# Optimization experiments

Measured on AMD Instinct MI355X. Metric: run time of the kernel, lower is better.

The kernel has to match this reference:

```python
import jax, jax.numpy as jnp
import numpy as np
from jax import lax

K = 3
STRIDE = 1
PAD = 1


def setup_inputs() -> dict:
    key = jax.random.key(0)
    k0, k1, k2, k3 = jax.random.split(key, 4)
    B, C, H, W, O = 8, 128, 64, 64, 128
    x = jax.random.normal(k0, (B, C, H, W), jnp.float32)
    # offset_conv: Conv2d(C, 2*K*K) - small init so sampled offsets stay moderate
    w_off = jax.random.normal(k1, (2 * K * K, C, K, K), jnp.float32) * 0.01
    b_off = jnp.zeros((2 * K * K,), jnp.float32)
    # deform_conv main weight, kaiming-ish scale
    w_def = jax.random.normal(k2, (O, C, K, K), jnp.float32) * (1.0 / np.sqrt(C * K * K))
    b_def = jax.random.normal(k3, (O,), jnp.float32) * 0.01
    return {"x": x, "w_off": w_off, "b_off": b_off, "w_def": w_def, "b_def": b_def}


def _conv2d(x, w, b, stride, pad):
    y = lax.conv_general_dilated(
        x, w, window_strides=(stride, stride), padding=[(pad, pad), (pad, pad)],
        dimension_numbers=("NCHW", "OIHW", "NCHW"))
    return y + b[None, :, None, None]


def _bilinear_sample(x, py, px):
    """x: [B,C,Hin,Win]; py,px: [B,KK,H,W] -> [B,C,KK,H,W] with zero padding."""
    B, C, Hin, Win = x.shape
    iy0f = jnp.floor(py)
    ix0f = jnp.floor(px)
    wy = py - iy0f  # grad of floor is 0, so d(wy)/d(py) = 1 (matches deform conv)
    wx = px - ix0f
    iy0 = iy0f.astype(jnp.int32)
    ix0 = ix0f.astype(jnp.int32)

    def gather(iy, ix):
        valid = (iy >= 0) & (iy < Hin) & (ix >= 0) & (ix < Win)
        iyc = jnp.clip(iy, 0, Hin - 1)
        ixc = jnp.clip(ix, 0, Win - 1)
        g = jax.vmap(lambda xb, a, b: xb[:, a, b])(x, iyc, ixc)  # [B,C,KK,H,W]
        return g * valid[:, None].astype(x.dtype)

    v00 = gather(iy0, ix0)
    v01 = gather(iy0, ix0 + 1)
    v10 = gather(iy0 + 1, ix0)
    v11 = gather(iy0 + 1, ix0 + 1)
    wy_ = wy[:, None]
    wx_ = wx[:, None]
    return (v00 * (1 - wy_) * (1 - wx_) + v01 * (1 - wy_) * wx_
            + v10 * wy_ * (1 - wx_) + v11 * wy_ * wx_)


def reference(x, w_off, b_off, w_def, b_def):
    B, C, H, W = x.shape
    O = w_def.shape[0]
    KK = K * K
    # 1) standard conv predicting offsets: [B, 2*KK, Hout, Wout]
    offsets = _conv2d(x, w_off, b_off, STRIDE, PAD)
    Hout, Wout = offsets.shape[2], offsets.shape[3]
    # torchvision layout: interleaved (dy, dx) per kernel tap
    off = offsets.reshape(B, KK, 2, Hout, Wout)
    off_y, off_x = off[:, :, 0], off[:, :, 1]  # [B,KK,Hout,Wout]
    # 2) base sampling grid per kernel tap
    kys, kxs = jnp.meshgrid(jnp.arange(K), jnp.arange(K), indexing="ij")
    kys = kys.reshape(KK).astype(jnp.float32)
    kxs = kxs.reshape(KK).astype(jnp.float32)
    hs = (jnp.arange(Hout) * STRIDE - PAD).astype(jnp.float32)
    ws = (jnp.arange(Wout) * STRIDE - PAD).astype(jnp.float32)
    base_y = hs[None, :, None] + kys[:, None, None]  # [KK,Hout,1]
    base_x = ws[None, None, :] + kxs[:, None, None]  # [KK,1,Wout]
    py = base_y[None] + off_y  # [B,KK,Hout,Wout]
    px = base_x[None] + off_x
    # 3) gather bilinear-sampled patches then dense contraction (im2col GEMM)
    sampled = _bilinear_sample(x, py, px)  # [B,C,KK,Hout,Wout]
    out = jnp.einsum("bckhw,ock->bohw", sampled, w_def.reshape(O, C, KK))
    return out + b_def[None, :, None, None]
```

## Files before the change

kernel.cpp:

```cpp
#include <hip/hip_runtime.h>

#define BB 8
#define CC 128
#define HH 64
#define WW 64
#define OO 128
#define NJ 18
#define HW 4096

typedef unsigned short u16;
typedef unsigned int u32;
typedef __attribute__((ext_vector_type(8))) __bf16 bf16x8;
typedef __attribute__((ext_vector_type(4))) float f32x4;

__device__ __forceinline__ u16 f2bf(float f) {
    u32 u = __float_as_uint(f);
    u += 0x7fffu + ((u >> 16) & 1u);
    return (u16)(u >> 16);
}
__device__ __forceinline__ float bflo(u32 u) { return __uint_as_float(u << 16); }
__device__ __forceinline__ float bfhi(u32 u) { return __uint_as_float(u & 0xffff0000u); }

__global__ __launch_bounds__(256)
void k_xT(const float* __restrict__ x, u16* __restrict__ xT) {
    __shared__ float tile[128][65];
    const int t = threadIdx.x;
    const int b = blockIdx.x >> 6;
    const int hw0 = (blockIdx.x & 63) << 6;
    const float* xb = x + (size_t)b * CC * HW + hw0;
    const int tw = t & 63, tc = t >> 6;
#pragma unroll
    for (int r = 0; r < 32; ++r) {
        int c = r * 4 + tc;
        tile[c][tw] = xb[c * HW + tw];
    }
    __syncthreads();
    const int seg = t & 15, hwl = t >> 4;
    u16* dst = xT + ((size_t)b * HW + hw0) * CC;
#pragma unroll
    for (int r = 0; r < 4; ++r) {
        int hw = hwl + r * 16;
        union { u16 u[8]; uint4 v; } p;
#pragma unroll
        for (int i = 0; i < 8; ++i) p.u[i] = f2bf(tile[seg * 8 + i][hw]);
        *(uint4*)&dst[hw * CC + seg * 8] = p.v;
    }
}

__global__ void k_prep(const float* __restrict__ w_def,
                       const float* __restrict__ w_off,
                       u16* __restrict__ wT, u16* __restrict__ wA) {
    int idx = blockIdx.x * 256 + threadIdx.x;
    if (idx < 9 * OO * CC) {
        int c = idx & 127, o = (idx >> 7) & 127, kk = idx >> 14;
        wT[idx] = f2bf(w_def[(o * CC + c) * 9 + kk]);
    }
    if (idx < 32 * 1152) {
        int k = idx % 1152, j = idx / 1152;
        int q = k >> 7, c = k & 127;
        wA[idx] = (j < NJ) ? f2bf(w_off[(j * CC + c) * 9 + q]) : (u16)0;
    }
}

__global__ __launch_bounds__(256, 2)
void k_off(const u16* __restrict__ xT, const u16* __restrict__ wA,
           const float* __restrict__ b_off, float* __restrict__ offs) {
    __shared__ u16 s_x[198 * 128];
    const int t = threadIdx.x, lane = t & 63, wv = t >> 6;
    const int posl = lane & 15, kg = lane >> 4;
    const int b = blockIdx.x >> 6, h = blockIdx.x & 63;

    for (int it = t; it < 3168; it += 256) {
        int seg = it & 15, pix = it >> 4;
        int r = pix / 66, wp = pix - r * 66;
        int y = h - 1 + r, w = wp - 1;
        uint4 v = make_uint4(0, 0, 0, 0);
        if (y >= 0 && y < HH && w >= 0 && w < WW)
            v = *(const uint4*)&xT[((size_t)(b * HW) + y * WW + w) * CC + seg * 8];
        *(uint4*)&s_x[pix * 128 + ((seg ^ (pix & 15)) * 8)] = v;
    }
    __syncthreads();

    f32x4 acc0 = {0.f, 0.f, 0.f, 0.f}, acc1 = {0.f, 0.f, 0.f, 0.f};
    for (int q = 0; q < 9; ++q) {
        int qy = q / 3, qx = q - qy * 3;
        int pix = qy * 66 + (wv * 16 + posl) + qx;
        int prow = pix * 128, pxor = pix & 15;
#pragma unroll
        for (int ki = 0; ki < 4; ++ki) {
            int ks = q * 4 + ki;
            int cidx = ki * 4 + kg;
            bf16x8 bfr = *(const bf16x8*)&s_x[prow + ((cidx ^ pxor) * 8)];
            bf16x8 a0 = *(const bf16x8*)&wA[posl * 1152 + ks * 32 + kg * 8];
            bf16x8 a1 = *(const bf16x8*)&wA[(16 + posl) * 1152 + ks * 32 + kg * 8];
            acc0 = __builtin_amdgcn_mfma_f32_16x16x32_bf16(a0, bfr, acc0, 0, 0, 0);
            acc1 = __builtin_amdgcn_mfma_f32_16x16x32_bf16(a1, bfr, acc1, 0, 0, 0);
        }
    }
    const int pos = wv * 16 + posl;
#pragma unroll
    for (int r = 0; r < 4; ++r) {
        int j = kg * 4 + r;
        offs[(b * NJ + j) * HW + h * WW + pos] = acc0[r] + b_off[j];
    }
#pragma unroll
    for (int r = 0; r < 4; ++r) {
        int j = 16 + kg * 4 + r;
        if (j < NJ) offs[(b * NJ + j) * HW + h * WW + pos] = acc1[r] + b_off[j];
    }
}

__global__ __launch_bounds__(256, 2)
void k_main(const u16* __restrict__ xT, const float* __restrict__ offs,
            const u16* __restrict__ wT, const float* __restrict__ b_def,
            float* __restrict__ out) {
    __shared__ u16    s_wt[128 * 128];
    __shared__ u16    s_samp[128 * 128];
    __shared__ float4 s_cw[128];
    __shared__ int4   s_co[128];

    const int t = threadIdx.x, lane = t & 63, wv = t >> 6;
    const int posl = lane & 15, rg = lane >> 4;
    const int b = blockIdx.x >> 5;
    const int h0 = (blockIdx.x & 31) << 1;
    const char* xb = (const char*)xT + (size_t)b * (HW * CC * 2);

    f32x4 acc[8][2];
#pragma unroll
    for (int mt = 0; mt < 8; ++mt) {
        acc[mt][0] = (f32x4){0.f, 0.f, 0.f, 0.f};
        acc[mt][1] = (f32x4){0.f, 0.f, 0.f, 0.f};
    }

    for (int kk = 0; kk < 9; ++kk) {
        if (t < 128) {
            int w = t & 63, hc = h0 + (t >> 6);
            int ky = kk / 3, kx = kk - ky * 3;
            int idy = (b * NJ + 2 * kk) * HW + hc * WW + w;
            float oy = offs[idy];
            float ox = offs[idy + HW];
            float py = (float)(hc - 1 + ky) + oy;
            float px = (float)(w - 1 + kx) + ox;
            float fy = floorf(py), fx = floorf(px);
            int iy0 = (int)fy, ix0 = (int)fx;
            float wy = py - fy, wx = px - fx;
            int iy1 = iy0 + 1, ix1 = ix0 + 1;
            float my0 = (iy0 >= 0 && iy0 < HH) ? 1.0f : 0.0f;
            float my1 = (iy1 >= 0 && iy1 < HH) ? 1.0f : 0.0f;
            float mx0 = (ix0 >= 0 && ix0 < WW) ? 1.0f : 0.0f;
            float mx1 = (ix1 >= 0 && ix1 < WW) ? 1.0f : 0.0f;
            int iy0c = min(max(iy0, 0), HH - 1), iy1c = min(max(iy1, 0), HH - 1);
            int ix0c = min(max(ix0, 0), WW - 1), ix1c = min(max(ix1, 0), WW - 1);
            float wy1 = 1.0f - wy, wx1 = 1.0f - wx;
            s_cw[t] = make_float4(my0 * mx0 * wy1 * wx1, my0 * mx1 * wy1 * wx,
                                  my1 * mx0 * wy  * wx1, my1 * mx1 * wy  * wx);
            s_co[t] = make_int4((iy0c * WW + ix0c) << 8, (iy0c * WW + ix1c) << 8,
                                (iy1c * WW + ix0c) << 8, (iy1c * WW + ix1c) << 8);
        }
        __syncthreads();

#pragma unroll
        for (int r = 0; r < 8; ++r) {
            int item = r * 256 + t;
            int o = item >> 4, sg = item & 15;
            *(uint4*)&s_wt[o * 128 + ((sg ^ (o & 15)) * 8)] =
                *(const uint4*)&wT[kk * (OO * CC) + item * 8];
        }
        {
            const int sg = t & 15;
            const char* base = xb + sg * 16;
#pragma unroll
            for (int r = 0; r < 8; ++r) {
                int pos = (t >> 4) + r * 16;
                float4 cw = s_cw[pos];
                int4 co = s_co[pos];
                uint4 q00 = *(const uint4*)(base + co.x);
                uint4 q01 = *(const uint4*)(base + co.y);
                uint4 q10 = *(const uint4*)(base + co.z);
                uint4 q11 = *(const uint4*)(base + co.w);
                const u32* u00 = (const u32*)&q00;
                const u32* u01 = (const u32*)&q01;
                const u32* u10 = (const u32*)&q10;
                const u32* u11 = (const u32*)&q11;
                union { u16 u[8]; uint4 v; } p;
#pragma unroll
                for (int i = 0; i < 4; ++i) {
                    float s0 = cw.x * bflo(u00[i]) + cw.y * bflo(u01[i])
                             + cw.z * bflo(u10[i]) + cw.w * bflo(u11[i]);
                    float s1 = cw.x * bfhi(u00[i]) + cw.y * bfhi(u01[i])
                             + cw.z * bfhi(u10[i]) + cw.w * bfhi(u11[i]);
                    p.u[2 * i]     = f2bf(s0);
                    p.u[2 * i + 1] = f2bf(s1);
                }
                *(uint4*)&s_samp[pos * 128 + ((sg ^ (pos & 15)) * 8)] = p.v;
            }
        }
        __syncthreads();

#pragma unroll
        for (int ct = 0; ct < 4; ++ct) {
            const int cidx = ct * 4 + rg;
            const int sw = (cidx ^ posl) * 8;
            bf16x8 bf0 = *(const bf16x8*)&s_samp[(2 * wv * 16 + posl) * 128 + sw];
            bf16x8 bf1 = *(const bf16x8*)&s_samp[((2 * wv + 1) * 16 + posl) * 128 + sw];
#pragma unroll
            for (int mt = 0; mt < 8; ++mt) {
                bf16x8 af = *(const bf16x8*)&s_wt[(mt * 16 + posl) * 128 + sw];
                acc[mt][0] = __builtin_amdgcn_mfma_f32_16x16x32_bf16(af, bf0, acc[mt][0], 0, 0, 0);
                acc[mt][1] = __builtin_amdgcn_mfma_f32_16x16x32_bf16(af, bf1, acc[mt][1], 0, 0, 0);
            }
        }
        __syncthreads();
    }

#pragma unroll
    for (int mt = 0; mt < 8; ++mt) {
#pragma unroll
        for (int j = 0; j < 2; ++j) {
            int pos = (2 * wv + j) * 16 + posl;
            int h = h0 + (pos >> 6), w = pos & 63;
#pragma unroll
            for (int r = 0; r < 4; ++r) {
                int o = mt * 16 + rg * 4 + r;
                out[((b * OO + o) * HH + h) * WW + w] = acc[mt][j][r] + b_def[o];
            }
        }
    }
}

extern "C" void kernel_launch(void* const* d_in, const int* in_sizes, int n_in,
                              void* d_out, int out_size, void* d_ws, size_t ws_size,
                              hipStream_t stream) {
    const float* x     = (const float*)d_in[0];
    const float* w_off = (const float*)d_in[1];
    const float* b_off = (const float*)d_in[2];
    const float* w_def = (const float*)d_in[3];
    const float* b_def = (const float*)d_in[4];
    float* out = (float*)d_out;

    float* offs = (float*)d_ws;
    u16*   xT   = (u16*)(offs + BB * NJ * HW);
    u16*   wT   = xT + (size_t)BB * HW * CC;
    u16*   wA   = wT + 9 * OO * CC;

    k_xT  <<<512, 256, 0, stream>>>(x, xT);
    k_prep<<<576, 256, 0, stream>>>(w_def, w_off, wT, wA);
    k_off <<<512, 256, 0, stream>>>(xT, wA, b_off, offs);
    k_main<<<256, 256, 0, stream>>>(xT, offs, wT, b_def, out);
}
```

Baseline: 139.4 us.

## Retile deformable conv to one row per block and compute sampling per lane

The main kernel now handles one output row (64 pixels) per block instead of two, doubling the grid to 512 blocks and raising launch bounds to 3 blocks per SM. Each lane computes its own bilinear coefficients inline, which removes the shared coefficient staging and one barrier per tap. The sample buffer is padded and relaid per channel segment. Separately, the transpose kernel changes its shared tile layout and packs bf16 pairs with a hardware conversion, and both offset and main kernels interleave batch in block index order to improve L2 locality. The trade-off is that the weight tile is reloaded to LDS for half as many pixels per block, doubling that traffic, and every wave recomputes the same sampling coefficients redundantly.

```diff
diff --git a/kernel.cpp b/kernel.cpp
--- a/kernel.cpp
+++ b/kernel.cpp
@@ -1,4 +1,5 @@
 #include <hip/hip_runtime.h>
+#include <hip/hip_bf16.h>
 
 #define BB 8
 #define CC 128
@@ -20,10 +21,15 @@
 }
 __device__ __forceinline__ float bflo(u32 u) { return __uint_as_float(u << 16); }
 __device__ __forceinline__ float bfhi(u32 u) { return __uint_as_float(u & 0xffff0000u); }
+__device__ __forceinline__ u32 pk2bf(float s0, float s1) {
+    union { __hip_bfloat162 h; u32 u; } cv;
+    cv.h = __float22bfloat162_rn(make_float2(s0, s1));
+    return cv.u;
+}
 
 __global__ __launch_bounds__(256)
 void k_xT(const float* __restrict__ x, u16* __restrict__ xT) {
-    __shared__ float tile[128][65];
+    __shared__ float tile[64][129];
     const int t = threadIdx.x;
     const int b = blockIdx.x >> 6;
     const int hw0 = (blockIdx.x & 63) << 6;
@@ -32,17 +38,18 @@
 #pragma unroll
     for (int r = 0; r < 32; ++r) {
         int c = r * 4 + tc;
-        tile[c][tw] = xb[c * HW + tw];
+        tile[tw][c] = xb[c * HW + tw];
     }
     __syncthreads();
-    const int seg = t & 15, hwl = t >> 4;
     u16* dst = xT + ((size_t)b * HW + hw0) * CC;
 #pragma unroll
     for (int r = 0; r < 4; ++r) {
-        int hw = hwl + r * 16;
-        union { u16 u[8]; uint4 v; } p;
-#pragma unroll
-        for (int i = 0; i < 8; ++i) p.u[i] = f2bf(tile[seg * 8 + i][hw]);
+        int item = t + (r << 8);
+        int seg = item & 15, hw = item >> 4;
+        union { u32 d[4]; uint4 v; } p;
+#pragma unroll
+        for (int i = 0; i < 4; ++i)
+            p.d[i] = pk2bf(tile[hw][seg * 8 + 2 * i], tile[hw][seg * 8 + 2 * i + 1]);
         *(uint4*)&dst[hw * CC + seg * 8] = p.v;
     }
 }
@@ -68,7 +75,7 @@
     __shared__ u16 s_x[198 * 128];
     const int t = threadIdx.x, lane = t & 63, wv = t >> 6;
     const int posl = lane & 15, kg = lane >> 4;
-    const int b = blockIdx.x >> 6, h = blockIdx.x & 63;
+    const int b = blockIdx.x & 7, h = blockIdx.x >> 3;
 
     for (int it = t; it < 3168; it += 256) {
         int seg = it & 15, pix = it >> 4;
@@ -110,55 +117,25 @@
     }
 }
 
-__global__ __launch_bounds__(256, 2)
+__global__ __launch_bounds__(256, 3)
 void k_main(const u16* __restrict__ xT, const float* __restrict__ offs,
             const u16* __restrict__ wT, const float* __restrict__ b_def,
             float* __restrict__ out) {
-    __shared__ u16    s_wt[128 * 128];
-    __shared__ u16    s_samp[128 * 128];
-    __shared__ float4 s_cw[128];
-    __shared__ int4   s_co[128];
+    __shared__ u16 s_wt[128 * 128];
+    __shared__ u16 s_samp[16 * 520];
 
     const int t = threadIdx.x, lane = t & 63, wv = t >> 6;
     const int posl = lane & 15, rg = lane >> 4;
-    const int b = blockIdx.x >> 5;
-    const int h0 = (blockIdx.x & 31) << 1;
+    const int b = blockIdx.x & 7;
+    const int h = blockIdx.x >> 3;
+    const int w = lane;
     const char* xb = (const char*)xT + (size_t)b * (HW * CC * 2);
 
-    f32x4 acc[8][2];
-#pragma unroll
-    for (int mt = 0; mt < 8; ++mt) {
-        acc[mt][0] = (f32x4){0.f, 0.f, 0.f, 0.f};
-        acc[mt][1] = (f32x4){0.f, 0.f, 0.f, 0.f};
-    }
+    f32x4 acc[8];
+#pragma unroll
+    for (int mt = 0; mt < 8; ++mt) acc[mt] = (f32x4){0.f, 0.f, 0.f, 0.f};
 
     for (int kk = 0; kk < 9; ++kk) {
-        if (t < 128) {
-            int w = t & 63, hc = h0 + (t >> 6);
-            int ky = kk / 3, kx = kk - ky * 3;
-            int idy = (b * NJ + 2 * kk) * HW + hc * WW + w;
-            float oy = offs[idy];
-            float ox = offs[idy + HW];
-            float py = (float)(hc - 1 + ky) + oy;
-            float px = (float)(w - 1 + kx) + ox;
-            float fy = floorf(py), fx = floorf(px);
-            int iy0 = (int)fy, ix0 = (int)fx;
-            float wy = py - fy, wx = px - fx;
-            int iy1 = iy0 + 1, ix1 = ix0 + 1;
-            float my0 = (iy0 >= 0 && iy0 < HH) ? 1.0f : 0.0f;
-            float my1 = (iy1 >= 0 && iy1 < HH) ? 1.0f : 0.0f;
-            float mx0 = (ix0 >= 0 && ix0 < WW) ? 1.0f : 0.0f;
-            float mx1 = (ix1 >= 0 && ix1 < WW) ? 1.0f : 0.0f;
-            int iy0c = min(max(iy0, 0), HH - 1), iy1c = min(max(iy1, 0), HH - 1);
-            int ix0c = min(max(ix0, 0), WW - 1), ix1c = min(max(ix1, 0), WW - 1);
-            float wy1 = 1.0f - wy, wx1 = 1.0f - wx;
-            s_cw[t] = make_float4(my0 * mx0 * wy1 * wx1, my0 * mx1 * wy1 * wx,
-                                  my1 * mx0 * wy  * wx1, my1 * mx1 * wy  * wx);
-            s_co[t] = make_int4((iy0c * WW + ix0c) << 8, (iy0c * WW + ix1c) << 8,
-                                (iy1c * WW + ix0c) << 8, (iy1c * WW + ix1c) << 8);
-        }
-        __syncthreads();
-
 #pragma unroll
         for (int r = 0; r < 8; ++r) {
             int item = r * 256 + t;
@@ -166,64 +143,72 @@
             *(uint4*)&s_wt[o * 128 + ((sg ^ (o & 15)) * 8)] =
                 *(const uint4*)&wT[kk * (OO * CC) + item * 8];
         }
-        {
-            const int sg = t & 15;
-            const char* base = xb + sg * 16;
-#pragma unroll
-            for (int r = 0; r < 8; ++r) {
-                int pos = (t >> 4) + r * 16;
-                float4 cw = s_cw[pos];
-                int4 co = s_co[pos];
-                uint4 q00 = *(const uint4*)(base + co.x);
-                uint4 q01 = *(const uint4*)(base + co.y);
-                uint4 q10 = *(const uint4*)(base + co.z);
-                uint4 q11 = *(const uint4*)(base + co.w);
-                const u32* u00 = (const u32*)&q00;
-                const u32* u01 = (const u32*)&q01;
-                const u32* u10 = (const u32*)&q10;
-                const u32* u11 = (const u32*)&q11;
-                union { u16 u[8]; uint4 v; } p;
-#pragma unroll
-                for (int i = 0; i < 4; ++i) {
-                    float s0 = cw.x * bflo(u00[i]) + cw.y * bflo(u01[i])
-                             + cw.z * bflo(u10[i]) + cw.w * bflo(u11[i]);
-                    float s1 = cw.x * bfhi(u00[i]) + cw.y * bfhi(u01[i])
-                             + cw.z * bfhi(u10[i]) + cw.w * bfhi(u11[i]);
-                    p.u[2 * i]     = f2bf(s0);
-                    p.u[2 * i + 1] = f2bf(s1);
-                }
-                *(uint4*)&s_samp[pos * 128 + ((sg ^ (pos & 15)) * 8)] = p.v;
+        int ky = kk / 3, kx = kk - ky * 3;
+        float oy = offs[(b * NJ + 2 * kk) * HW + h * WW + w];
+        float ox = offs[(b * NJ + 2 * kk + 1) * HW + h * WW + w];
+        float py = (float)(h - 1 + ky) + oy;
+        float px = (float)(w - 1 + kx) + ox;
+        float fy = floorf(py), fx = floorf(px);
+        int iy0 = (int)fy, ix0 = (int)fx;
+        float wy = py - fy, wx = px - fx;
+        int iy1 = iy0 + 1, ix1 = ix0 + 1;
+        float my0 = (iy0 >= 0 && iy0 < HH) ? 1.0f : 0.0f;
+        float my1 = (iy1 >= 0 && iy1 < HH) ? 1.0f : 0.0f;
+        float mx0 = (ix0 >= 0 && ix0 < WW) ? 1.0f : 0.0f;
+        float mx1 = (ix1 >= 0 && ix1 < WW) ? 1.0f : 0.0f;
+        int iy0c = min(max(iy0, 0), HH - 1), iy1c = min(max(iy1, 0), HH - 1);
+        int ix0c = min(max(ix0, 0), WW - 1), ix1c = min(max(ix1, 0), WW - 1);
+        float wy1 = 1.0f - wy, wx1 = 1.0f - wx;
+        float cwx = my0 * mx0 * wy1 * wx1, cwy = my0 * mx1 * wy1 * wx;
+        float cwz = my1 * mx0 * wy * wx1,  cww = my1 * mx1 * wy * wx;
+        int cox = (iy0c * WW + ix0c) << 8, coy = (iy0c * WW + ix1c) << 8;
+        int coz = (iy1c * WW + ix0c) << 8, cow = (iy1c * WW + ix1c) << 8;
+
+#pragma unroll
+        for (int j = 0; j < 4; ++j) {
+            const int seg = 4 * wv + j;
+            const char* base = xb + seg * 16;
+            uint4 q00 = *(const uint4*)(base + cox);
+            uint4 q01 = *(const uint4*)(base + coy);
+            uint4 q10 = *(const uint4*)(base + coz);
+            uint4 q11 = *(const uint4*)(base + cow);
+            const u32* u00 = (const u32*)&q00;
+            const u32* u01 = (const u32*)&q01;
+            const u32* u10 = (const u32*)&q10;
+            const u32* u11 = (const u32*)&q11;
+            union { u32 d[4]; uint4 v; } p;
+#pragma unroll
+            for (int i = 0; i < 4; ++i) {
+                float s0 = cwx * bflo(u00[i]) + cwy * bflo(u01[i])
+                         + cwz * bflo(u10[i]) + cww * bflo(u11[i]);
+                float s1 = cwx * bfhi(u00[i]) + cwy * bfhi(u01[i])
+                         + cwz * bfhi(u10[i]) + cww * bfhi(u11[i]);
+                p.d[i] = pk2bf(s0, s1);
             }
+            *(uint4*)&s_samp[seg * 520 + lane * 8] = p.v;
         }
         __syncthreads();
 
 #pragma unroll
         for (int ct = 0; ct < 4; ++ct) {
             const int cidx = ct * 4 + rg;
-            const int sw = (cidx ^ posl) * 8;
-            bf16x8 bf0 = *(const bf16x8*)&s_samp[(2 * wv * 16 + posl) * 128 + sw];
-            bf16x8 bf1 = *(const bf16x8*)&s_samp[((2 * wv + 1) * 16 + posl) * 128 + sw];
+            bf16x8 bfr = *(const bf16x8*)&s_samp[cidx * 520 + (wv * 16 + posl) * 8];
 #pragma unroll
             for (int mt = 0; mt < 8; ++mt) {
-                bf16x8 af = *(const bf16x8*)&s_wt[(mt * 16 + posl) * 128 + sw];
-                acc[mt][0] = __builtin_amdgcn_mfma_f32_16x16x32_bf16(af, bf0, acc[mt][0], 0, 0, 0);
-                acc[mt][1] = __builtin_amdgcn_mfma_f32_16x16x32_bf16(af, bf1, acc[mt][1], 0, 0, 0);
+                bf16x8 af = *(const bf16x8*)&s_wt[(mt * 16 + posl) * 128 + ((cidx ^ posl) * 8)];
+                acc[mt] = __builtin_amdgcn_mfma_f32_16x16x32_bf16(af, bfr, acc[mt], 0, 0, 0);
             }
         }
         __syncthreads();
     }
 
+    const int wout = wv * 16 + posl;
 #pragma unroll
     for (int mt = 0; mt < 8; ++mt) {
 #pragma unroll
-        for (int j = 0; j < 2; ++j) {
-            int pos = (2 * wv + j) * 16 + posl;
-            int h = h0 + (pos >> 6), w = pos & 63;
-#pragma unroll
-            for (int r = 0; r < 4; ++r) {
-                int o = mt * 16 + rg * 4 + r;
-                out[((b * OO + o) * HH + h) * WW + w] = acc[mt][j][r] + b_def[o];
-            }
+        for (int r = 0; r < 4; ++r) {
+            int o = mt * 16 + rg * 4 + r;
+            out[((b * OO + o) * HH + h) * WW + wout] = acc[mt][r] + b_def[o];
         }
     }
 }
@@ -246,5 +231,5 @@
     k_xT  <<<512, 256, 0, stream>>>(x, xT);
     k_prep<<<576, 256, 0, stream>>>(w_def, w_off, wT, wA);
     k_off <<<512, 256, 0, stream>>>(xT, wA, b_off, offs);
-    k_main<<<256, 256, 0, stream>>>(xT, offs, wT, b_def, out);
-}
+    k_main<<<512, 256, 0, stream>>>(xT, offs, wT, b_def, out);
+}
```

Measured after the change: 159.7 us. 1.15x slower.
